# Kernel optimization log

Measured on AMD Instinct MI355X. Metric: run time of the kernel, lower is better.

The kernel has to match this reference:

```python
import jax, jax.numpy as jnp
import numpy as np

GAMMA = 0.002  # Gaussian kernel bandwidth (init_kwargs)


def setup_inputs() -> dict:
    key = jax.random.key(0)
    k1, k2 = jax.random.split(key)
    x = jax.random.normal(k1, (4096, 512), dtype=jnp.float32)   # queries [B, D]
    sv = jax.random.normal(k2, (8192, 512), dtype=jnp.float32)  # centers [N, D]
    return {"x": x, "sv": sv}


def reference(x, sv):
    # Gaussian (RBF) kernel matrix: K[b, n] = exp(-gamma * ||x_b - sv_n||^2)
    # original chunked broadcast-subtract-square loop (same math, fused).
    x2 = jnp.sum(x * x, axis=-1)            # [B]
    s2 = jnp.sum(sv * sv, axis=-1)          # [N]
    cross = jnp.einsum('bd,nd->bn', x, sv)  # [B, N]
    d2 = x2[:, None] + s2[None, :] - 2.0 * cross
    return jnp.exp(-GAMMA * d2)
```

## Files before the change

### kernel.cpp

```cpp
#include <hip/hip_runtime.h>
#include <stdint.h>

#define GAMMA 0.002f
#define MDIM 4096
#define NDIM 8192
#define KDIM 512

typedef short v8s __attribute__((ext_vector_type(8)));
typedef float v4f __attribute__((ext_vector_type(4)));

__device__ __forceinline__ unsigned short f32_to_bf16_rne(float f) {
    union { float f; uint32_t u; } v; v.f = f;
    uint32_t u = v.u;
    return (unsigned short)((u + 0x7fffu + ((u >> 16) & 1u)) >> 16);
}

__device__ __forceinline__ void gl_lds16(const void* g, void* l) {
    __builtin_amdgcn_global_load_lds(
        (const __attribute__((address_space(1))) uint32_t*)g,
        (__attribute__((address_space(3))) uint32_t*)l, 16, 0, 0);
}

__global__ __launch_bounds__(256) void convert_rows(
    const float* __restrict__ in, unsigned short* __restrict__ outb,
    float* __restrict__ neg_g_sq) {
    int row = blockIdx.x;
    const float* src = in + (size_t)row * KDIM;
    unsigned short* dst = outb + (size_t)row * KDIM;
    int t = threadIdx.x;
    float2 f = ((const float2*)src)[t];
    ushort2 b;
    b.x = f32_to_bf16_rne(f.x);
    b.y = f32_to_bf16_rne(f.y);
    ((ushort2*)dst)[t] = b;
    float s = f.x * f.x + f.y * f.y;
    #pragma unroll
    for (int off = 32; off > 0; off >>= 1) s += __shfl_down(s, off, 64);
    __shared__ float red[4];
    if ((t & 63) == 0) red[t >> 6] = s;
    __syncthreads();
    if (t == 0) neg_g_sq[row] = -GAMMA * (red[0] + red[1] + red[2] + red[3]);
}

__global__ __launch_bounds__(256, 3) void rbf_gemm(
    const unsigned short* __restrict__ A,
    const unsigned short* __restrict__ B,
    const float* __restrict__ arow,
    const float* __restrict__ ccol,
    float* __restrict__ out) {

    __shared__ __align__(16) char smem[50176];

    const int tid  = threadIdx.x;
    const int lane = tid & 63;
    const int wave = tid >> 6;
    const int wm   = wave >> 1;
    const int wn   = wave & 1;

    const int bid = blockIdx.x;
    const int xcd = bid & 7;
    const int idx = bid >> 3;
    const int mt  = ((xcd & 1) << 4) | (idx & 15);
    const int nt  = ((xcd >> 1) << 4) | (idx >> 4);
    const int row0 = mt << 7;
    const int col0 = nt << 7;

    const int rS  = tid >> 2;
    const int cSw = ((tid & 3) << 4) ^ ((rS & 3) << 4);
    const char* aS = (const char*)A + ((size_t)(row0 + rS) << 10) + cSw;
    const char* bS = (const char*)B + ((size_t)(col0 + rS) << 10) + cSw;
    char* dA = smem + tid * 16;
    char* dB = smem + 8192 + tid * 16;

    #define STAGE(t)                                                          \
      do {                                                                    \
        const int _b = ((t) % 3) * 16384;                                     \
        const char* _sa = aS + (t) * 64;                                      \
        const char* _sb = bS + (t) * 64;                                      \
        gl_lds16(_sa,          dA + _b);                                      \
        gl_lds16(_sa + 65536,  dA + _b + 4096);                               \
        gl_lds16(_sb,          dB + _b);                                      \
        gl_lds16(_sb + 65536,  dB + _b + 4096);                               \
      } while (0)

    const int q   = lane >> 4;
    const int l15 = lane & 15;
    const int ra0 = wm * 64 + l15;
    const int aOff = ra0 * 64 + (((q << 4)) ^ ((ra0 & 3) << 4));
    const int rb0 = wn * 64 + l15;
    const int bOff = 8192 + rb0 * 64 + (((q << 4)) ^ ((rb0 & 3) << 4));

    v4f acc[4][4];
    #pragma unroll
    for (int i = 0; i < 4; ++i)
        #pragma unroll
        for (int j = 0; j < 4; ++j) acc[i][j] = (v4f)0.0f;

    STAGE(0); STAGE(1);
    if (tid < 128) ((float*)(smem + 49152))[tid] = arow[row0 + tid];
    else           ((float*)(smem + 49664))[tid - 128] = ccol[col0 + tid - 128];
    asm volatile("s_waitcnt vmcnt(4)" ::: "memory");
    __builtin_amdgcn_s_barrier();

    #pragma unroll
    for (int t = 0; t < 16; ++t) {
        if (t + 2 < 16) STAGE(t + 2);
        const int bo = (t % 3) * 16384;
        v8s af[4], bf[4];
        #pragma unroll
        for (int i = 0; i < 4; ++i) af[i] = *(const v8s*)(smem + bo + aOff + i * 1024);
        #pragma unroll
        for (int j = 0; j < 4; ++j) bf[j] = *(const v8s*)(smem + bo + bOff + j * 1024);
        __builtin_amdgcn_s_setprio(1);
        #pragma unroll
        for (int i = 0; i < 4; ++i)
            #pragma unroll
            for (int j = 0; j < 4; ++j)
                acc[i][j] = __builtin_amdgcn_mfma_f32_16x16x32_bf16(
                    bf[j], af[i], acc[i][j], 0, 0, 0);
        __builtin_amdgcn_s_setprio(0);
        if (t < 14)      asm volatile("s_waitcnt vmcnt(4)" ::: "memory");
        else if (t == 14) asm volatile("s_waitcnt vmcnt(0)" ::: "memory");
        __builtin_amdgcn_s_barrier();
    }
    #undef STAGE

    const float tg = 2.0f * GAMMA;
    const float* sbr = (const float*)(smem + 49152);
    const float* sbc = (const float*)(smem + 49664);
    #pragma unroll
    for (int i = 0; i < 4; ++i) {
        const float ra = sbr[wm * 64 + i * 16 + l15];
        #pragma unroll
        for (int j = 0; j < 4; ++j) {
            #pragma unroll
            for (int v = 0; v < 4; ++v) {
                const int c_l = wn * 64 + j * 16 + (q << 2) + v;
                acc[i][j][v] = __expf(fmaf(tg, acc[i][j][v], ra + sbc[c_l]));
            }
        }
    }

    float* tb = (float*)smem;
    #pragma unroll
    for (int ch = 0; ch < 2; ++ch) {
        if (wm == ch) {
            #pragma unroll
            for (int i = 0; i < 4; ++i) {
                const int rl = i * 16 + l15;
                #pragma unroll
                for (int j = 0; j < 4; ++j) {
                    const int g = wn * 16 + j * 4 + q;
                    *(v4f*)&tb[rl * 128 + ((g ^ (rl & 31)) << 2)] = acc[i][j];
                }
            }
        }
        __syncthreads();
        #pragma unroll
        for (int rr = 0; rr < 8; ++rr) {
            const int rl = wave * 16 + (rr << 1) + (lane >> 5);
            v4f val = *(const v4f*)&tb[rl * 128 + (((lane & 31) ^ (rl & 31)) << 2)];
            *(v4f*)(out + (size_t)(row0 + ch * 64 + rl) * NDIM + col0 +
                    ((lane & 31) << 2)) = val;
        }
        __syncthreads();
    }
}

extern "C" void kernel_launch(void* const* d_in, const int* in_sizes, int n_in,
                              void* d_out, int out_size, void* d_ws, size_t ws_size,
                              hipStream_t stream) {
    const float* x  = (const float*)d_in[0];
    const float* sv = (const float*)d_in[1];
    float* out = (float*)d_out;

    unsigned short* xb  = (unsigned short*)d_ws;
    unsigned short* svb = xb + (size_t)MDIM * KDIM;
    float* arow = (float*)(svb + (size_t)NDIM * KDIM);
    float* ccol = arow + MDIM;

    hipLaunchKernelGGL(convert_rows, dim3(MDIM), dim3(256), 0, stream, x, xb, arow);
    hipLaunchKernelGGL(convert_rows, dim3(NDIM), dim3(256), 0, stream, sv, svb, ccol);
    hipLaunchKernelGGL(rbf_gemm, dim3((MDIM / 128) * (NDIM / 128)), dim3(256), 0,
                       stream, xb, svb, arow, ccol, out);
}
```

Before: 183.7 us.

## Use chunk-major LDS tile layout and store epilogue results directly to global

The shared-memory staging layout changes from swizzled row-major to k-chunk-major. Each thread now loads one 16-byte chunk of a row, and each wave's MFMA operand reads become contiguous 256-byte runs with no XOR swizzle. The epilogue drops the LDS transpose buffer and its barriers, and each lane writes its 4-float results straight to global memory. This removes LDS traffic and synchronisation in the epilogue. In exchange, global stores become narrower per row (64-byte segments instead of full 512-byte rows) and global loads are less coalesced per instruction.

```diff
diff --git a/kernel.cpp b/kernel.cpp
--- a/kernel.cpp
+++ b/kernel.cpp
@@ -65,10 +65,10 @@
     const int row0 = mt << 7;
     const int col0 = nt << 7;
 
-    const int rS  = tid >> 2;
-    const int cSw = ((tid & 3) << 4) ^ ((rS & 3) << 4);
-    const char* aS = (const char*)A + ((size_t)(row0 + rS) << 10) + cSw;
-    const char* bS = (const char*)B + ((size_t)(col0 + rS) << 10) + cSw;
+    const int rT = tid & 127;
+    const int cT = tid >> 7;
+    const char* aS = (const char*)A + ((size_t)(row0 + rT) << 10) + (cT << 4);
+    const char* bS = (const char*)B + ((size_t)(col0 + rT) << 10) + (cT << 4);
     char* dA = smem + tid * 16;
     char* dB = smem + 8192 + tid * 16;
 
@@ -77,18 +77,16 @@
         const int _b = ((t) % 3) * 16384;                                     \
         const char* _sa = aS + (t) * 64;                                      \
         const char* _sb = bS + (t) * 64;                                      \
-        gl_lds16(_sa,          dA + _b);                                      \
-        gl_lds16(_sa + 65536,  dA + _b + 4096);                               \
-        gl_lds16(_sb,          dB + _b);                                      \
-        gl_lds16(_sb + 65536,  dB + _b + 4096);                               \
+        gl_lds16(_sa,       dA + _b);                                         \
+        gl_lds16(_sa + 32,  dA + _b + 4096);                                  \
+        gl_lds16(_sb,       dB + _b);                                         \
+        gl_lds16(_sb + 32,  dB + _b + 4096);                                  \
       } while (0)
 
     const int q   = lane >> 4;
     const int l15 = lane & 15;
-    const int ra0 = wm * 64 + l15;
-    const int aOff = ra0 * 64 + (((q << 4)) ^ ((ra0 & 3) << 4));
-    const int rb0 = wn * 64 + l15;
-    const int bOff = 8192 + rb0 * 64 + (((q << 4)) ^ ((rb0 & 3) << 4));
+    const int aOff = q * 2048 + wm * 1024 + l15 * 16;
+    const int bOff = 8192 + q * 2048 + wn * 1024 + l15 * 16;
 
     v4f acc[4][4];
     #pragma unroll
@@ -108,9 +106,9 @@
         const int bo = (t % 3) * 16384;
         v8s af[4], bf[4];
         #pragma unroll
-        for (int i = 0; i < 4; ++i) af[i] = *(const v8s*)(smem + bo + aOff + i * 1024);
+        for (int i = 0; i < 4; ++i) af[i] = *(const v8s*)(smem + bo + aOff + i * 256);
         #pragma unroll
-        for (int j = 0; j < 4; ++j) bf[j] = *(const v8s*)(smem + bo + bOff + j * 1024);
+        for (int j = 0; j < 4; ++j) bf[j] = *(const v8s*)(smem + bo + bOff + j * 256);
         __builtin_amdgcn_s_setprio(1);
         #pragma unroll
         for (int i = 0; i < 4; ++i)
@@ -130,40 +128,19 @@
     const float* sbc = (const float*)(smem + 49664);
     #pragma unroll
     for (int i = 0; i < 4; ++i) {
-        const float ra = sbr[wm * 64 + i * 16 + l15];
+        const int r_l = wm * 64 + i * 16 + l15;
+        const float ra = sbr[r_l];
+        float* gp = out + (size_t)(row0 + r_l) * NDIM + col0 + wn * 64 + (q << 2);
         #pragma unroll
         for (int j = 0; j < 4; ++j) {
+            v4f o;
             #pragma unroll
             for (int v = 0; v < 4; ++v) {
                 const int c_l = wn * 64 + j * 16 + (q << 2) + v;
-                acc[i][j][v] = __expf(fmaf(tg, acc[i][j][v], ra + sbc[c_l]));
+                o[v] = __expf(fmaf(tg, acc[i][j][v], ra + sbc[c_l]));
             }
+            *(v4f*)(gp + j * 16) = o;
         }
-    }
-
-    float* tb = (float*)smem;
-    #pragma unroll
-    for (int ch = 0; ch < 2; ++ch) {
-        if (wm == ch) {
-            #pragma unroll
-            for (int i = 0; i < 4; ++i) {
-                const int rl = i * 16 + l15;
-                #pragma unroll
-                for (int j = 0; j < 4; ++j) {
-                    const int g = wn * 16 + j * 4 + q;
-                    *(v4f*)&tb[rl * 128 + ((g ^ (rl & 31)) << 2)] = acc[i][j];
-                }
-            }
-        }
-        __syncthreads();
-        #pragma unroll
-        for (int rr = 0; rr < 8; ++rr) {
-            const int rl = wave * 16 + (rr << 1) + (lane >> 5);
-            v4f val = *(const v4f*)&tb[rl * 128 + (((lane & 31) ^ (rl & 31)) << 2)];
-            *(v4f*)(out + (size_t)(row0 + ch * 64 + rl) * NDIM + col0 +
-                    ((lane & 31) << 2)) = val;
-        }
-        __syncthreads();
     }
 }
 
```

After: 217.0 us. 1.18x slower.
